# Performance work log

Measured on AMD Instinct MI355X. Metric: run time of the kernel, lower is better.

## Reference

```python
import jax, jax.numpy as jnp
import numpy as np

D_MODEL = 512
N_HEADS = 8
HEAD_DIM = D_MODEL // N_HEADS
BATCH = 2
SEQ = 4096
MAX_SEQ = 4096


def _rope_tables(max_len, dim):
    # freqs = 1/10000^(arange(0,dim,2)/dim); outer(t, freqs); polar -> cos/sin
    inv = 1.0 / (10000.0 ** (np.arange(0, dim, 2, dtype=np.float32) / dim))
    t = np.arange(max_len, dtype=np.float32)
    ang = np.outer(t, inv)  # [max_len, dim/2]
    return jnp.asarray(np.cos(ang)), jnp.asarray(np.sin(ang))


def _apply_rope(x, cos, sin):
    # x: [B, S, H, Hd]; complex-pair rotation over last dim pairs
    B, S, H, Hd = x.shape
    xr = x.reshape(B, S, H, Hd // 2, 2)
    xe, xo = xr[..., 0], xr[..., 1]
    c = cos[:S][None, :, None, :]  # [1,S,1,Hd/2]
    s = sin[:S][None, :, None, :]
    re = xe * c - xo * s
    im = xe * s + xo * c
    return jnp.stack([re, im], axis=-1).reshape(B, S, H, Hd)


def setup_inputs() -> dict:
    key = jax.random.key(0)
    kx, kq, kk, kv, ko = jax.random.split(key, 5)
    std = 1.0 / np.sqrt(D_MODEL)
    return {
        "x": jax.random.normal(kx, (BATCH, SEQ, D_MODEL), dtype=jnp.float32),
        "Wq": jax.random.normal(kq, (D_MODEL, D_MODEL), dtype=jnp.float32) * std,
        "Wk": jax.random.normal(kk, (D_MODEL, D_MODEL), dtype=jnp.float32) * std,
        "Wv": jax.random.normal(kv, (D_MODEL, D_MODEL), dtype=jnp.float32) * std,
        "Wo": jax.random.normal(ko, (D_MODEL, D_MODEL), dtype=jnp.float32) * std,
    }


def reference(x, Wq, Wk, Wv, Wo):
    B, S, D = x.shape
    cos, sin = _rope_tables(MAX_SEQ, HEAD_DIM)
    # nn.Linear: y = x @ W.T
    q = (x @ Wq.T).reshape(B, S, N_HEADS, HEAD_DIM)
    k = (x @ Wk.T).reshape(B, S, N_HEADS, HEAD_DIM)
    v = (x @ Wv.T).reshape(B, S, N_HEADS, HEAD_DIM)
    q = _apply_rope(q, cos, sin)
    k = _apply_rope(k, cos, sin)
    scale = HEAD_DIM ** (-0.5)
    # [B,H,S,S]
    scores = jnp.einsum("bshd,bthd->bhst", q, k) * scale
    causal = jnp.tril(jnp.ones((S, S), dtype=bool))
    scores = jnp.where(causal[None, None], scores, -jnp.inf)
    attn = jax.nn.softmax(scores, axis=-1)
    out = jnp.einsum("bhst,bthd->bshd", attn, v).reshape(B, S, D)
    return out @ Wo.T
```

## Files before the change

### kernel.cpp

```cpp
#include <hip/hip_runtime.h>
#include <hip/hip_bf16.h>
#include <math.h>

#define D_MODEL 512
#define N_HEADS 8
#define HEAD_DIM 64
#define BATCH 2
#define SEQ 4096
#define M_ROWS (BATCH*SEQ)

typedef __attribute__((ext_vector_type(8))) short short8;
typedef __attribute__((ext_vector_type(4))) float f32x4;

__device__ inline short f2bf(float f) {
  union { float f; unsigned u; } v; v.f = f;
  unsigned u = v.u;
  unsigned r = u + 0x7FFFu + ((u >> 16) & 1u);
  return (short)(r >> 16);
}
__device__ inline float bf2f(short s) {
  union { unsigned u; float f; } v; v.u = ((unsigned)(unsigned short)s) << 16;
  return v.f;
}

__device__ inline void gll16(const void* g, void* l) {
  __builtin_amdgcn_global_load_lds(
      (const __attribute__((address_space(1))) unsigned int*)g,
      (__attribute__((address_space(3))) unsigned int*)l, 16, 0, 0);
}

__global__ void prep_kernel(const float* __restrict__ x,
                            const float* __restrict__ Wq,
                            const float* __restrict__ Wk,
                            const float* __restrict__ Wv,
                            const float* __restrict__ Wo,
                            short* __restrict__ xb,
                            short* __restrict__ Wqkv,
                            short* __restrict__ Wob,
                            float* __restrict__ cosT,
                            float* __restrict__ sinT) {
  int i = blockIdx.x * blockDim.x + threadIdx.x;
  if (i < M_ROWS * D_MODEL) xb[i] = f2bf(x[i]);
  if (i < 3 * D_MODEL * D_MODEL) {
    int t = i >> 18;
    int r = i & 262143;
    const float* W = (t == 0) ? Wq : ((t == 1) ? Wk : Wv);
    Wqkv[i] = f2bf(W[r]);
  }
  if (i < D_MODEL * D_MODEL) Wob[i] = f2bf(Wo[i]);
  if (i < SEQ * 32) {
    int s = i >> 5, p = i & 31;
    float e = (float)(2 * p) * (1.0f / 64.0f);
    float inv = powf(10000.0f, -e);
    float ang = (float)s * inv;
    float sv, cv;
    sincosf(ang, &sv, &cv);
    cosT[i] = cv; sinT[i] = sv;
  }
}

template<int MODE>
__global__ __launch_bounds__(256) void gemm_kernel(const short* __restrict__ A,
                                                   const short* __restrict__ B,
                                                   float* __restrict__ out_f,
                                                   short* __restrict__ Qb,
                                                   short* __restrict__ Kb,
                                                   short* __restrict__ Vb,
                                                   const float* __restrict__ cosT,
                                                   const float* __restrict__ sinT) {
  __shared__ short smem[128 * 72 * 2];
  short (*As)[72] = (short(*)[72])smem;
  short (*Bs)[72] = (short(*)[72])(smem + 128 * 72);
  short (*Cs)[136] = (short(*)[136])smem;

  const int m0 = blockIdx.x * 128;
  const int n0 = blockIdx.y * 128;
  const int tid = threadIdx.x;
  const int lane = tid & 63, wid = tid >> 6;
  const int wm = wid >> 1, wn = wid & 1;
  const int l15 = lane & 15, g = lane >> 4;
  const int Kdim = 512;

  f32x4 acc[4][4] = {};

  for (int kt = 0; kt < Kdim; kt += 64) {
    __syncthreads();
    for (int it = 0; it < 4; ++it) {
      int c = it * 256 + tid;
      int row = c >> 3, col = (c & 7) << 3;
      *(short8*)&As[row][col] = *(const short8*)&A[(m0 + row) * Kdim + kt + col];
      *(short8*)&Bs[row][col] = *(const short8*)&B[(n0 + row) * Kdim + kt + col];
    }
    __syncthreads();
    for (int kk = 0; kk < 64; kk += 32) {
      short8 a[4], b[4];
      for (int mi = 0; mi < 4; ++mi)
        a[mi] = *(const short8*)&As[wm * 64 + mi * 16 + l15][kk + (g << 3)];
      for (int ni = 0; ni < 4; ++ni)
        b[ni] = *(const short8*)&Bs[wn * 64 + ni * 16 + l15][kk + (g << 3)];
      for (int mi = 0; mi < 4; ++mi)
        for (int ni = 0; ni < 4; ++ni)
          acc[mi][ni] = __builtin_amdgcn_mfma_f32_16x16x32_bf16(a[mi], b[ni], acc[mi][ni], 0, 0, 0);
    }
  }

  if (MODE == 1) {
    for (int mi = 0; mi < 4; ++mi)
      for (int ni = 0; ni < 4; ++ni)
        for (int r = 0; r < 4; ++r) {
          int row_g = m0 + wm * 64 + mi * 16 + (g << 2) + r;
          int col_g = n0 + wn * 64 + ni * 16 + l15;
          out_f[row_g * 512 + col_g] = acc[mi][ni][r];
        }
    return;
  }

  const int t_blk = n0 >> 9;
  __syncthreads();

  if (t_blk < 2) {
    const float qs = (t_blk == 0) ? 0.18033688011112042f : 1.0f;
    for (int mi = 0; mi < 4; ++mi)
      for (int ni = 0; ni < 4; ++ni)
        for (int r = 0; r < 4; ++r) {
          int lrow = wm * 64 + mi * 16 + (g << 2) + r;
          int ss = (m0 + lrow) & 4095;
          int d = (n0 + wn * 64 + ni * 16 + l15) & 63;
          int p = d >> 1;
          float c = cosT[ss * 32 + p], s = sinT[ss * 32 + p];
          float v = acc[mi][ni][r];
          float partner = __shfl_xor(v, 1);
          float res = (l15 & 1) ? (v * c + partner * s) : (v * c - partner * s);
          Cs[lrow][wn * 64 + ni * 16 + l15] = f2bf(res * qs);
        }
  } else {
    for (int mi = 0; mi < 4; ++mi)
      for (int ni = 0; ni < 4; ++ni)
        for (int r = 0; r < 4; ++r)
          Cs[wm * 64 + mi * 16 + (g << 2) + r][wn * 64 + ni * 16 + l15] =
              f2bf(acc[mi][ni][r]);
  }
  __syncthreads();

  if (t_blk < 2) {
    short* dst = (t_blk == 0) ? Qb : Kb;
#pragma unroll
    for (int it = 0; it < 8; ++it) {
      int row = (tid >> 4) + (it << 4);
      int colb = (tid & 15) << 3;
      short8 vv = *(const short8*)&Cs[row][colb];
      int row_g = m0 + row;
      int ss = row_g & 4095, bb = row_g >> 12;
      int cc = (n0 + colb) & 511;
      int h = cc >> 6, d = cc & 63;
      *(short8*)&dst[(((bb << 3) + h) * SEQ + ss) * 64 + d] = vv;
    }
  } else {
#pragma unroll
    for (int it = 0; it < 8; ++it) {
      int c = tid & 127;
      int sb = ((tid >> 7) << 3) + (it << 4);
      short8 o8;
#pragma unroll
      for (int j = 0; j < 8; ++j) o8[j] = Cs[sb + j][c];
      int row_g0 = m0 + sb;
      int ss = row_g0 & 4095, bb = row_g0 >> 12;
      int cc = (n0 + c) & 511;
      int h = cc >> 6, d = cc & 63;
      *(short8*)&Vb[((long)(((bb << 3) + h) * 64 + d)) * SEQ + ss] = o8;
    }
  }
}

__global__ __launch_bounds__(512, 4) void attn_kernel(const short* __restrict__ Q,
                                                      const short* __restrict__ K,
                                                      const short* __restrict__ Vt,
                                                      short* __restrict__ O) {
  __shared__ short Ks[2][64 * 64];
  __shared__ short Vs[2][64 * 64];
  __shared__ short P_lds[8][16][72];

  const int o = blockIdx.x;
  const int j = o >> 4;
  const int bh = o & 15;
  const int tile = (o < 256) ? (31 - j) : (j - 16);

  const int tid = threadIdx.x, lane = tid & 63, w = tid >> 6;
  const int l15 = lane & 15, g = lane >> 4;
  const long base = (long)bh * SEQ * 64;
  const long baseV = (long)bh * 64 * SEQ;
  const int bb = bh >> 3, h = bh & 7;

  const int srow = tid >> 3;
  const int sc16k = (tid & 7) ^ (srow & 7);
  short* ldsSegK0 = &Ks[0][(tid >> 6) << 9];
  short* ldsSegK1 = &Ks[1][(tid >> 6) << 9];
  short* ldsSegV0 = &Vs[0][(tid >> 6) << 9];
  short* ldsSegV1 = &Vs[1][(tid >> 6) << 9];

  const int q0 = (tile << 7) + (w << 4);
  const int nc = 2 * tile + 2;

  short8 aq0 = *(const short8*)&Q[base + (long)(q0 + l15) * 64 + (g << 3)];
  short8 aq1 = *(const short8*)&Q[base + (long)(q0 + l15) * 64 + 32 + (g << 3)];

  f32x4 o_acc[4] = {};
  float m_r[4], l_r[4];
#pragma unroll
  for (int r = 0; r < 4; ++r) { m_r[r] = -__builtin_inff(); l_r[r] = 0.f; }

  gll16(&K[base + (long)srow * 64 + sc16k * 8], ldsSegK0);
  gll16(&Vt[baseV + (long)srow * SEQ + sc16k * 8], ldsSegV0);

  for (int c = 0; c < nc; ++c) {
    const int kv0 = c << 6;
    const int bi = c & 1;
    __syncthreads();
    if (c + 1 < nc) {
      const int nkv = (c + 1) << 6;
      short* dK = (bi ? ldsSegK0 : ldsSegK1);
      short* dV = (bi ? ldsSegV0 : ldsSegV1);
      gll16(&K[base + (long)(nkv + srow) * 64 + sc16k * 8], dK);
      gll16(&Vt[baseV + (long)srow * SEQ + nkv + sc16k * 8], dV);
    }
    if (kv0 > q0) continue;

    f32x4 sf[4] = {};
    __builtin_amdgcn_s_setprio(1);
#pragma unroll
    for (int f = 0; f < 4; ++f) {
      int row = f * 16 + l15, sw = row & 7;
      short8 bk0 = *(const short8*)&Ks[bi][row * 64 + ((g) ^ sw) * 8];
      short8 bk1 = *(const short8*)&Ks[bi][row * 64 + ((4 + g) ^ sw) * 8];
      sf[f] = __builtin_amdgcn_mfma_f32_16x16x32_bf16(aq0, bk0, sf[f], 0, 0, 0);
      sf[f] = __builtin_amdgcn_mfma_f32_16x16x32_bf16(aq1, bk1, sf[f], 0, 0, 0);
    }
    __builtin_amdgcn_s_setprio(0);
    if (kv0 == (q0 & ~63)) {
#pragma unroll
      for (int f = 0; f < 4; ++f) {
        int kvc = kv0 + f * 16 + l15;
#pragma unroll
        for (int r = 0; r < 4; ++r) {
          int qrow = q0 + (g << 2) + r;
          if (kvc > qrow) sf[f][r] = -__builtin_inff();
        }
      }
    }

    float pm[4];
#pragma unroll
    for (int r = 0; r < 4; ++r)
      pm[r] = fmaxf(fmaxf(sf[0][r], sf[1][r]), fmaxf(sf[2][r], sf[3][r]));
#pragma unroll
    for (int off = 1; off < 16; off <<= 1)
#pragma unroll
      for (int r = 0; r < 4; ++r)
        pm[r] = fmaxf(pm[r], __shfl_xor(pm[r], off));

    float pr[4][4], rs[4];
#pragma unroll
    for (int r = 0; r < 4; ++r) {
      float mn = fmaxf(m_r[r], pm[r]);
      float alpha = exp2f(m_r[r] - mn);
      m_r[r] = mn;
      l_r[r] *= alpha;
      float s0 = 0.f;
#pragma unroll
      for (int f = 0; f < 4; ++f) {
        float pv = exp2f(sf[f][r] - mn);
        pr[f][r] = pv;
        s0 += pv;
      }
      rs[r] = s0;
#pragma unroll
      for (int db = 0; db < 4; ++db) o_acc[db][r] *= alpha;
    }
#pragma unroll
    for (int off = 1; off < 16; off <<= 1)
#pragma unroll
      for (int r = 0; r < 4; ++r)
        rs[r] += __shfl_xor(rs[r], off);
#pragma unroll
    for (int r = 0; r < 4; ++r) l_r[r] += rs[r];

#pragma unroll
    for (int f = 0; f < 4; ++f)
#pragma unroll
      for (int r = 0; r < 4; ++r)
        P_lds[w][(g << 2) + r][f * 16 + l15] = f2bf(pr[f][r]);

    short8 pa0 = *(const short8*)&P_lds[w][l15][(g << 3)];
    short8 pa1 = *(const short8*)&P_lds[w][l15][32 + (g << 3)];

    __builtin_amdgcn_s_setprio(1);
#pragma unroll
    for (int kk = 0; kk < 2; ++kk) {
      short8 pa = kk ? pa1 : pa0;
#pragma unroll
      for (int db = 0; db < 4; ++db) {
        int row = db * 16 + l15, sw = row & 7;
        short8 bv = *(const short8*)&Vs[bi][row * 64 + ((kk * 4 + g) ^ sw) * 8];
        o_acc[db] = __builtin_amdgcn_mfma_f32_16x16x32_bf16(pa, bv, o_acc[db], 0, 0, 0);
      }
    }
    __builtin_amdgcn_s_setprio(0);
  }

#pragma unroll
  for (int db = 0; db < 4; ++db)
#pragma unroll
    for (int r = 0; r < 4; ++r) {
      int s_g = q0 + (g << 2) + r;
      float v = o_acc[db][r] / l_r[r];
      O[((long)(bb * SEQ + s_g)) * 512 + h * 64 + db * 16 + l15] = f2bf(v);
    }
}

extern "C" void kernel_launch(void* const* d_in, const int* in_sizes, int n_in,
                              void* d_out, int out_size, void* d_ws, size_t ws_size,
                              hipStream_t stream) {
  const float* x  = (const float*)d_in[0];
  const float* Wq = (const float*)d_in[1];
  const float* Wk = (const float*)d_in[2];
  const float* Wv = (const float*)d_in[3];
  const float* Wo = (const float*)d_in[4];

  char* ws = (char*)d_ws;
  size_t off = 0;
  auto alloc = [&](size_t bytes) {
    void* p = ws + off;
    off += (bytes + 255) & ~(size_t)255;
    return p;
  };
  short* xb   = (short*)alloc((size_t)M_ROWS * 512 * 2);
  short* Wqkv = (short*)alloc((size_t)1536 * 512 * 2);
  short* Wob  = (short*)alloc((size_t)512 * 512 * 2);
  float* cosT = (float*)alloc((size_t)SEQ * 32 * 4);
  float* sinT = (float*)alloc((size_t)SEQ * 32 * 4);
  short* Qb   = (short*)alloc((size_t)16 * SEQ * 64 * 2);
  short* Kb   = (short*)alloc((size_t)16 * SEQ * 64 * 2);
  short* Vt   = (short*)alloc((size_t)16 * SEQ * 64 * 2);
  short* Obuf = (short*)alloc((size_t)M_ROWS * 512 * 2);

  prep_kernel<<<16384, 256, 0, stream>>>(x, Wq, Wk, Wv, Wo, xb, Wqkv, Wob, cosT, sinT);
  gemm_kernel<0><<<dim3(64, 12), 256, 0, stream>>>(xb, Wqkv, nullptr, Qb, Kb, Vt, cosT, sinT);
  attn_kernel<<<512, 512, 0, stream>>>(Qb, Kb, Vt, Obuf);
  gemm_kernel<1><<<dim3(64, 4), 256, 0, stream>>>(Obuf, Wob, (float*)d_out, nullptr, nullptr, nullptr, nullptr, nullptr);
}
```

Before: 252.5 us.

## Vectorize bf16 prep conversion and add lazy softmax rescaling in attention

The prep kernel now converts eight floats per thread with float4 loads and short8 stores, and launches an eighth as many blocks. This cuts per-element instruction and launch overhead in the conversion pass. In the attention loop, the running max and rescale of the output accumulator are skipped whenever every row's block max stays within 8 (log2 units) of the current max, checked wave-wide with __all. The per-iteration cross-lane row-sum shuffles move to a single reduction after the loop. This removes shuffle and exp work from the inner loop, at the cost of a divergence-free branch and unnormalized values that can grow by up to about 2^8.

New measurement: 208.1 us. 17.6% less time.

```diff
diff --git a/kernel.cpp b/kernel.cpp
--- a/kernel.cpp
+++ b/kernel.cpp
@@ -29,6 +29,16 @@
       (__attribute__((address_space(3))) unsigned int*)l, 16, 0, 0);
 }
 
+__device__ inline short8 cvt8(float4 a, float4 b) {
+  short8 o;
+  o[0] = f2bf(a.x); o[1] = f2bf(a.y); o[2] = f2bf(a.z); o[3] = f2bf(a.w);
+  o[4] = f2bf(b.x); o[5] = f2bf(b.y); o[6] = f2bf(b.z); o[7] = f2bf(b.w);
+  return o;
+}
+
+#define XOCT (M_ROWS*D_MODEL/8)
+#define WOCT (3*D_MODEL*D_MODEL/8)
+#define OOCT (D_MODEL*D_MODEL/8)
 __global__ void prep_kernel(const float* __restrict__ x,
                             const float* __restrict__ Wq,
                             const float* __restrict__ Wk,
@@ -40,14 +50,24 @@
                             float* __restrict__ cosT,
                             float* __restrict__ sinT) {
   int i = blockIdx.x * blockDim.x + threadIdx.x;
-  if (i < M_ROWS * D_MODEL) xb[i] = f2bf(x[i]);
-  if (i < 3 * D_MODEL * D_MODEL) {
-    int t = i >> 18;
-    int r = i & 262143;
+  if (i < XOCT) {
+    float4 a = *(const float4*)&x[i * 8];
+    float4 b = *(const float4*)&x[i * 8 + 4];
+    *(short8*)&xb[i * 8] = cvt8(a, b);
+  }
+  if (i < WOCT) {
+    int e = i * 8;
+    int t = e >> 18, r = e & 262143;
     const float* W = (t == 0) ? Wq : ((t == 1) ? Wk : Wv);
-    Wqkv[i] = f2bf(W[r]);
-  }
-  if (i < D_MODEL * D_MODEL) Wob[i] = f2bf(Wo[i]);
+    float4 a = *(const float4*)&W[r];
+    float4 b = *(const float4*)&W[r + 4];
+    *(short8*)&Wqkv[e] = cvt8(a, b);
+  }
+  if (i < OOCT) {
+    float4 a = *(const float4*)&Wo[i * 8];
+    float4 b = *(const float4*)&Wo[i * 8 + 4];
+    *(short8*)&Wob[i * 8] = cvt8(a, b);
+  }
   if (i < SEQ * 32) {
     int s = i >> 5, p = i & 31;
     float e = (float)(2 * p) * (1.0f / 64.0f);
@@ -248,41 +268,41 @@
       }
     }
 
-    float pm[4];
+    float pmx[4];
 #pragma unroll
     for (int r = 0; r < 4; ++r)
-      pm[r] = fmaxf(fmaxf(sf[0][r], sf[1][r]), fmaxf(sf[2][r], sf[3][r]));
-#pragma unroll
-    for (int off = 1; off < 16; off <<= 1)
-#pragma unroll
-      for (int r = 0; r < 4; ++r)
-        pm[r] = fmaxf(pm[r], __shfl_xor(pm[r], off));
-
-    float pr[4][4], rs[4];
-#pragma unroll
-    for (int r = 0; r < 4; ++r) {
-      float mn = fmaxf(m_r[r], pm[r]);
-      float alpha = exp2f(m_r[r] - mn);
-      m_r[r] = mn;
-      l_r[r] *= alpha;
-      float s0 = 0.f;
+      pmx[r] = fmaxf(fmaxf(sf[0][r], sf[1][r]), fmaxf(sf[2][r], sf[3][r]));
+    bool ok = (pmx[0] <= m_r[0] + 8.f) && (pmx[1] <= m_r[1] + 8.f) &&
+              (pmx[2] <= m_r[2] + 8.f) && (pmx[3] <= m_r[3] + 8.f);
+    if (!__all(ok)) {
+      float pm[4];
+#pragma unroll
+      for (int r = 0; r < 4; ++r) pm[r] = pmx[r];
+#pragma unroll
+      for (int off = 1; off < 16; off <<= 1)
+#pragma unroll
+        for (int r = 0; r < 4; ++r)
+          pm[r] = fmaxf(pm[r], __shfl_xor(pm[r], off));
+#pragma unroll
+      for (int r = 0; r < 4; ++r) {
+        float mn = fmaxf(m_r[r], pm[r]);
+        float alpha = exp2f(m_r[r] - mn);
+        m_r[r] = mn;
+        l_r[r] *= alpha;
+#pragma unroll
+        for (int db = 0; db < 4; ++db) o_acc[db][r] *= alpha;
+      }
+    }
+
+    float pr[4][4];
+#pragma unroll
+    for (int r = 0; r < 4; ++r)
 #pragma unroll
       for (int f = 0; f < 4; ++f) {
-        float pv = exp2f(sf[f][r] - mn);
+        float pv = exp2f(sf[f][r] - m_r[r]);
         pr[f][r] = pv;
-        s0 += pv;
+        l_r[r] += pv;
       }
-      rs[r] = s0;
-#pragma unroll
-      for (int db = 0; db < 4; ++db) o_acc[db][r] *= alpha;
-    }
-#pragma unroll
-    for (int off = 1; off < 16; off <<= 1)
-#pragma unroll
-      for (int r = 0; r < 4; ++r)
-        rs[r] += __shfl_xor(rs[r], off);
-#pragma unroll
-    for (int r = 0; r < 4; ++r) l_r[r] += rs[r];
 
 #pragma unroll
     for (int f = 0; f < 4; ++f)
@@ -306,6 +326,12 @@
     }
     __builtin_amdgcn_s_setprio(0);
   }
+
+#pragma unroll
+  for (int off = 1; off < 16; off <<= 1)
+#pragma unroll
+    for (int r = 0; r < 4; ++r)
+      l_r[r] += __shfl_xor(l_r[r], off);
 
 #pragma unroll
   for (int db = 0; db < 4; ++db)
@@ -343,7 +369,7 @@
   short* Vt   = (short*)alloc((size_t)16 * SEQ * 64 * 2);
   short* Obuf = (short*)alloc((size_t)M_ROWS * 512 * 2);
 
-  prep_kernel<<<16384, 256, 0, stream>>>(x, Wq, Wk, Wv, Wo, xb, Wqkv, Wob, cosT, sinT);
+  prep_kernel<<<2048, 256, 0, stream>>>(x, Wq, Wk, Wv, Wo, xb, Wqkv, Wob, cosT, sinT);
   gemm_kernel<0><<<dim3(64, 12), 256, 0, stream>>>(xb, Wqkv, nullptr, Qb, Kb, Vt, cosT, sinT);
   attn_kernel<<<512, 512, 0, stream>>>(Qb, Kb, Vt, Obuf);
   gemm_kernel<1><<<dim3(64, 4), 256, 0, stream>>>(Obuf, Wob, (float*)d_out, nullptr, nullptr, nullptr, nullptr, nullptr);
```
